# Kernel tuning notes

Measured on AMD Instinct MI355X. Metric: run time of the kernel, lower is better.

Reference implementation:

```python
import jax, jax.numpy as jnp
import numpy as np

N = 4096          # nodes (= Mamba sequence length)
E_EDGES = 65536   # edges
D = 512           # dim_h (= d_inner, expand=1)
NEXP = 4          # num_experts (cfg.model.num_experts)
DSTATE = 16
DCONV = 4
DTRANK = 32       # ceil(D/16)
EPS = 1e-5


def _silu(x):
    return x * jax.nn.sigmoid(x)


def _bn(h, g, b):
    # BatchNorm1d over node axis (batch statistics)
    mu = h.mean(0)
    var = h.var(0)
    return (h - mu) * jax.lax.rsqrt(var + EPS) * g + b


def _mamba(u, in_w, conv_w, conv_b, x_w, dt_w, dt_b, A_log, Dp, out_w):
    # u: [L, D] single-sequence Mamba(d_model=D, d_state=16, d_conv=4, expand=1)
    L = u.shape[0]
    xz = u @ in_w                      # [L, 2D]
    xc, z = xz[:, :D], xz[:, D:]
    xp = jnp.pad(xc, ((DCONV - 1, 0), (0, 0)))
    xconv = conv_b
    for k in range(DCONV):             # depthwise causal conv, tiny fixed loop
        xconv = xconv + conv_w[:, k] * xp[k:k + L]
    xs = _silu(xconv)                  # [L, D]
    dbc = xs @ x_w                     # [L, DTRANK + 2*DSTATE]
    dt = jax.nn.softplus(dbc[:, :DTRANK] @ dt_w + dt_b)          # [L, D]
    Bm = dbc[:, DTRANK:DTRANK + DSTATE]                          # [L, S]
    Cm = dbc[:, DTRANK + DSTATE:]                                # [L, S]
    A = -jnp.exp(A_log)                                          # [D, S]
    dA = jnp.exp(dt[:, :, None] * A[None])                       # [L, D, S]
    dBu = dt[:, :, None] * Bm[:, None, :] * xs[:, :, None]       # [L, D, S]

    def step(hprev, inp):
        dA_t, dBu_t, C_t = inp
        hn = dA_t * hprev + dBu_t
        return hn, (hn * C_t[None, :]).sum(-1)

    _, ys = jax.lax.scan(step, jnp.zeros((D, DSTATE), u.dtype), (dA, dBu, Cm))
    y = ys + Dp * xs
    return (y * _silu(z)) @ out_w      # [L, D]


def setup_inputs() -> dict:
    key = jax.random.key(0)
    ks = jax.random.split(key, 24)
    s = 1.0 / np.sqrt(D)
    inp = {}
    inp['x'] = jax.random.normal(ks[0], (N, D), jnp.float32)
    inp['edge_index'] = jax.random.randint(ks[1], (2, E_EDGES), 0, N)
    inp['edge_attr'] = jax.random.normal(ks[2], (E_EDGES, D), jnp.float32)
    # GINE nn: Linear(D,D) -> ReLU -> Linear(D,D)
    inp['gin_w1'] = jax.random.normal(ks[3], (D, D)) * s
    inp['gin_b1'] = jnp.zeros((D,))
    inp['gin_w2'] = jax.random.normal(ks[4], (D, D)) * s
    inp['gin_b2'] = jnp.zeros((D,))
    # BatchNorms
    inp['bn1l_g'] = jnp.ones((D,)); inp['bn1l_b'] = jnp.zeros((D,))
    inp['bn1a_g'] = jnp.ones((D,)); inp['bn1a_b'] = jnp.zeros((D,))
    inp['bn2_g'] = jnp.ones((D,)); inp['bn2_b'] = jnp.zeros((D,))
    # gating MLP [D, D//2, NEXP]
    inp['gate_w1'] = jax.random.normal(ks[5], (D, D // 2)) * s
    inp['gate_b1'] = jnp.zeros((D // 2,))
    inp['gate_w2'] = jax.random.normal(ks[6], (D // 2, NEXP)) * (1.0 / np.sqrt(D // 2))
    inp['gate_b2'] = jnp.zeros((NEXP,))
    # stacked per-expert Mamba params
    inp['in_w'] = jax.random.normal(ks[7], (NEXP, D, 2 * D)) * s
    inp['conv_w'] = jax.random.normal(ks[8], (NEXP, D, DCONV)) * 0.5
    inp['conv_b'] = jnp.zeros((NEXP, D))
    inp['x_w'] = jax.random.normal(ks[9], (NEXP, D, DTRANK + 2 * DSTATE)) * s
    inp['dt_w'] = jax.random.normal(ks[10], (NEXP, DTRANK, D)) * (1.0 / np.sqrt(DTRANK))
    inp['dt_b'] = jax.random.normal(ks[11], (NEXP, D)) * 0.1 - 4.0
    A0 = jnp.log(jnp.arange(1, DSTATE + 1, dtype=jnp.float32))
    inp['A_log'] = jnp.broadcast_to(A0, (NEXP, D, DSTATE)).copy()
    inp['Dp'] = jnp.ones((NEXP, D))
    inp['out_w'] = jax.random.normal(ks[12], (NEXP, D, D)) * s
    # FFN
    inp['ff_w1'] = jax.random.normal(ks[13], (D, 2 * D)) * s
    inp['ff_b1'] = jnp.zeros((2 * D,))
    inp['ff_w2'] = jax.random.normal(ks[14], (2 * D, D)) * (1.0 / np.sqrt(2 * D))
    inp['ff_b2'] = jnp.zeros((D,))
    return inp


def reference(x, edge_index, edge_attr,
              gin_w1, gin_b1, gin_w2, gin_b2,
              bn1l_g, bn1l_b, bn1a_g, bn1a_b, bn2_g, bn2_b,
              gate_w1, gate_b1, gate_w2, gate_b2,
              in_w, conv_w, conv_b, x_w, dt_w, dt_b, A_log, Dp, out_w,
              ff_w1, ff_b1, ff_w2, ff_b2):
    h_in = x
    src, dst = edge_index[0], edge_index[1]
    # local GINEConv: nn(x + sum_j relu(x_j + e_ji))
    msg = jax.nn.relu(x[src] + edge_attr)                      # [E, D]
    aggr = jax.ops.segment_sum(msg, dst, num_segments=N)       # [N, D]
    h_local = jax.nn.relu((x + aggr) @ gin_w1 + gin_b1) @ gin_w2 + gin_b2
    h_local = _bn(h_in + h_local, bn1l_g, bn1l_b)
    # gated mixture of Mamba experts
    gate = jax.nn.softmax(jax.nn.relu(x @ gate_w1 + gate_b1) @ gate_w2 + gate_b2, axis=-1)  # [N, NEXP]
    ys = jax.vmap(_mamba, in_axes=(None, 0, 0, 0, 0, 0, 0, 0, 0, 0))(
        x, in_w, conv_w, conv_b, x_w, dt_w, dt_b, A_log, Dp, out_w)  # [NEXP, N, D]
    h_attn = jnp.einsum('ne,end->nd', gate, ys)
    h_attn = _bn(h_in + h_attn, bn1a_g, bn1a_b)
    # fuse + FFN
    h = h_local + h_attn
    ff = jax.nn.relu(h @ ff_w1 + ff_b1) @ ff_w2 + ff_b2
    return _bn(h + ff, bn2_g, bn2_b)
```

## Files before the change

kernel.cpp:

```cpp
#include <hip/hip_runtime.h>
#include <hip/hip_bf16.h>
#include <math.h>

#define N_NODES 4096
#define E_EDGE 65536
#define D 512
#define NEXP 4
#define DSTATE 16
#define DCONV 4
#define DTRANK 32
#define EPS 1e-5f
#define LCHUNK 32
#define NCHUNK (N_NODES / LCHUNK)

typedef __hip_bfloat16 bf16;
typedef short bf16x8 __attribute__((ext_vector_type(8)));
typedef float f32x4 __attribute__((ext_vector_type(4)));
typedef unsigned short u16x4 __attribute__((ext_vector_type(4)));

__device__ __forceinline__ float siluf(float x) { return x / (1.f + __expf(-x)); }
__device__ __forceinline__ float softplusf(float x) {
  return (x > 20.f) ? x : log1pf(__expf(x));
}
__device__ __forceinline__ unsigned short f2bf(float v) {
  bf16 b = __float2bfloat16(v);
  return *reinterpret_cast<unsigned short*>(&b);
}
__device__ __forceinline__ float bfu2f(unsigned short u) {
  bf16 b;
  *reinterpret_cast<unsigned short*>(&b) = u;
  return __bfloat162float(b);
}

__device__ __forceinline__ void gload16(const void* g, void* l) {
  __builtin_amdgcn_global_load_lds(
      (const __attribute__((address_space(1))) void*)g,
      (__attribute__((address_space(3))) void*)l, 16, 0, 0);
}

template <int FN, int EPI, bool STATS>
__global__ __launch_bounds__(256, 2) void mm_k(
    const bf16* __restrict__ A, int lda, long sA,
    const bf16* __restrict__ Bt, int ldb, long sB,
    const float* __restrict__ bias,
    float* __restrict__ Cf, bf16* __restrict__ Cb, int ldc, long sC, int K,
    const float* __restrict__ part, float* __restrict__ sacc) {
  constexpr int BN = FN * 32;
  __shared__ __align__(16) bf16 As[2][128 * 32];
  __shared__ __align__(16) bf16 Bs[2][BN * 32];
  const int z = blockIdx.z;
  A += (size_t)z * sA;
  Bt += (size_t)z * sB;
  const int tid = threadIdx.x;
  const int w = tid >> 6, l = tid & 63;
  const int wr = w >> 1, wc = w & 1;
  const int bm = blockIdx.y * 128, bn = blockIdx.x * BN;

  f32x4 acc[4][FN];
#pragma unroll
  for (int i = 0; i < 4; ++i)
#pragma unroll
    for (int j = 0; j < FN; ++j) acc[i][j] = 0.f;

  const int srow = l >> 2, schunk = l & 3;
  const bf16* gA = A + (size_t)(bm + w * 16 + srow) * lda + schunk * 8;
  const bf16* gB = Bt + (size_t)(bn + w * 16 + srow) * ldb + schunk * 8;

  const int ar = wr * 64 + (l & 15);
  const int br = wc * FN * 16 + (l & 15);
  const int kb = l >> 4;

  auto stage = [&](int b, int k0) {
    gload16(gA + k0, As[b] + w * 512);
    gload16(gA + k0 + (size_t)64 * lda, As[b] + 64 * 32 + w * 512);
    gload16(gB + k0, Bs[b] + w * 512);
    if (FN == 4) gload16(gB + k0 + (size_t)64 * ldb, Bs[b] + 64 * 32 + w * 512);
  };

  stage(0, 0);
  __syncthreads();
  int cur = 0;
  for (int k0 = 0; k0 < K; k0 += 32) {
    if (k0 + 32 < K) stage(cur ^ 1, k0 + 32);
    const bf16x8* Ap = (const bf16x8*)As[cur];
    const bf16x8* Bp = (const bf16x8*)Bs[cur];
    bf16x8 af[4], bfr[FN];
#pragma unroll
    for (int i = 0; i < 4; ++i) af[i] = Ap[(ar + i * 16) * 4 + kb];
#pragma unroll
    for (int j = 0; j < FN; ++j) bfr[j] = Bp[(br + j * 16) * 4 + kb];
#pragma unroll
    for (int i = 0; i < 4; ++i)
#pragma unroll
      for (int j = 0; j < FN; ++j)
        acc[i][j] = __builtin_amdgcn_mfma_f32_16x16x32_bf16(bfr[j], af[i], acc[i][j], 0, 0, 0);
    __syncthreads();
    cur ^= 1;
  }

  if (Cf) Cf += (size_t)z * sC;
  if (Cb) Cb += (size_t)z * sC;
  const int r0 = bm + wr * 64 + (l & 15);
  const int cb0 = bn + wc * FN * 16 + ((l >> 4) << 2);
  f32x4 ssum[FN], ssq[FN];
  if (STATS) {
#pragma unroll
    for (int j = 0; j < FN; ++j) { ssum[j] = 0.f; ssq[j] = 0.f; }
  }
#pragma unroll
  for (int i = 0; i < 4; ++i) {
    const int row = r0 + i * 16;
#pragma unroll
    for (int j = 0; j < FN; ++j) {
      const int col = cb0 + j * 16;
      f32x4 v = acc[i][j];
      if (bias) v += *(const f32x4*)&bias[col];
      if (EPI == 1) {
#pragma unroll
        for (int r = 0; r < 4; ++r) v[r] = fmaxf(v[r], 0.f);
      }
      if (Cf) *(f32x4*)&Cf[(size_t)row * ldc + col] = v;
      if (Cb) {
        u16x4 u;
#pragma unroll
        for (int r = 0; r < 4; ++r) u[r] = f2bf(v[r]);
        *(u16x4*)&Cb[(size_t)row * ldc + col] = u;
      }
      if (STATS) {
        f32x4 p = *(const f32x4*)&part[(size_t)row * ldc + col];
        f32x4 t = v + p;
        ssum[j] += t;
        ssq[j] += t * t;
      }
    }
  }
  if (STATS) {
#pragma unroll
    for (int m = 1; m < 16; m <<= 1) {
#pragma unroll
      for (int j = 0; j < FN; ++j)
#pragma unroll
        for (int r = 0; r < 4; ++r) {
          ssum[j][r] += __shfl_xor(ssum[j][r], m);
          ssq[j][r] += __shfl_xor(ssq[j][r], m);
        }
    }
    if ((l & 15) == 0) {
#pragma unroll
      for (int j = 0; j < FN; ++j)
#pragma unroll
        for (int r = 0; r < 4; ++r) {
          atomicAdd(&sacc[cb0 + j * 16 + r], ssum[j][r]);
          atomicAdd(&sacc[512 + cb0 + j * 16 + r], ssq[j][r]);
        }
    }
  }
}

struct MmArgs {
  const bf16* A[4];
  const bf16* Bt[4];
  const float* bias[4];
  float* Cf[4];
  bf16* Cb[4];
  const float* part[4];
  float* sacc[4];
  long sA[4], sB[4], sC[4];
  int lda[4], ldb[4], ldc[4], K[4], epi[4], stats[4], gx[4], cum[4];
};
__global__ __launch_bounds__(256, 2) void mgemm_k(MmArgs a) {
  __shared__ __align__(16) bf16 As[2][128 * 32];
  __shared__ __align__(16) bf16 Bs[2][64 * 32];
  int b = blockIdx.x;
  int i = 0;
  while (b >= a.cum[i]) ++i;
  int local = b - (i ? a.cum[i - 1] : 0);
  const int perz = a.gx[i] * 32;
  const int z = local / perz;
  const int rem = local - z * perz;
  const int by = rem / a.gx[i];
  const int bx = rem - by * a.gx[i];
  const int lda = a.lda[i], ldb = a.ldb[i], ldc = a.ldc[i], K = a.K[i];
  const bf16* A = a.A[i] + (size_t)z * a.sA[i];
  const bf16* Bt = a.Bt[i] + (size_t)z * a.sB[i];

  const int tid = threadIdx.x;
  const int w = tid >> 6, l = tid & 63;
  const int wr = w >> 1, wc = w & 1;
  const int bm = by * 128, bn = bx * 64;

  f32x4 acc[4][2];
#pragma unroll
  for (int p = 0; p < 4; ++p)
#pragma unroll
    for (int j = 0; j < 2; ++j) acc[p][j] = 0.f;

  const int srow = l >> 2, schunk = l & 3;
  const bf16* gA = A + (size_t)(bm + w * 16 + srow) * lda + schunk * 8;
  const bf16* gB = Bt + (size_t)(bn + w * 16 + srow) * ldb + schunk * 8;

  const int ar = wr * 64 + (l & 15);
  const int br = wc * 32 + (l & 15);
  const int kb = l >> 4;

  auto stage = [&](int bb, int k0) {
    gload16(gA + k0, As[bb] + w * 512);
    gload16(gA + k0 + (size_t)64 * lda, As[bb] + 64 * 32 + w * 512);
    gload16(gB + k0, Bs[bb] + w * 512);
  };

  stage(0, 0);
  __syncthreads();
  int cur = 0;
  for (int k0 = 0; k0 < K; k0 += 32) {
    if (k0 + 32 < K) stage(cur ^ 1, k0 + 32);
    const bf16x8* Ap = (const bf16x8*)As[cur];
    const bf16x8* Bp = (const bf16x8*)Bs[cur];
    bf16x8 af[4], bfr[2];
#pragma unroll
    for (int p = 0; p < 4; ++p) af[p] = Ap[(ar + p * 16) * 4 + kb];
#pragma unroll
    for (int j = 0; j < 2; ++j) bfr[j] = Bp[(br + j * 16) * 4 + kb];
#pragma unroll
    for (int p = 0; p < 4; ++p)
#pragma unroll
      for (int j = 0; j < 2; ++j)
        acc[p][j] = __builtin_amdgcn_mfma_f32_16x16x32_bf16(bfr[j], af[p], acc[p][j], 0, 0, 0);
    __syncthreads();
    cur ^= 1;
  }

  float* Cf = a.Cf[i] ? a.Cf[i] + (size_t)z * a.sC[i] : nullptr;
  bf16* Cb = a.Cb[i] ? a.Cb[i] + (size_t)z * a.sC[i] : nullptr;
  const float* bias = a.bias[i];
  const int epi = a.epi[i], stats = a.stats[i];
  const int r0 = bm + wr * 64 + (l & 15);
  const int cb0 = bn + wc * 32 + ((l >> 4) << 2);
  f32x4 ssum[2], ssq[2];
  ssum[0] = 0.f; ssum[1] = 0.f; ssq[0] = 0.f; ssq[1] = 0.f;
#pragma unroll
  for (int p = 0; p < 4; ++p) {
    const int row = r0 + p * 16;
#pragma unroll
    for (int j = 0; j < 2; ++j) {
      const int col = cb0 + j * 16;
      f32x4 v = acc[p][j];
      if (bias) v += *(const f32x4*)&bias[col];
      if (epi == 1) {
#pragma unroll
        for (int r = 0; r < 4; ++r) v[r] = fmaxf(v[r], 0.f);
      }
      if (Cf) *(f32x4*)&Cf[(size_t)row * ldc + col] = v;
      if (Cb) {
        u16x4 u;
#pragma unroll
        for (int r = 0; r < 4; ++r) u[r] = f2bf(v[r]);
        *(u16x4*)&Cb[(size_t)row * ldc + col] = u;
      }
      if (stats) {
        f32x4 pp = *(const f32x4*)&a.part[i][(size_t)row * ldc + col];
        f32x4 t = v + pp;
        ssum[j] += t;
        ssq[j] += t * t;
      }
    }
  }
  if (stats) {
#pragma unroll
    for (int m = 1; m < 16; m <<= 1) {
#pragma unroll
      for (int j = 0; j < 2; ++j)
#pragma unroll
        for (int r = 0; r < 4; ++r) {
          ssum[j][r] += __shfl_xor(ssum[j][r], m);
          ssq[j][r] += __shfl_xor(ssq[j][r], m);
        }
    }
    if ((l & 15) == 0) {
#pragma unroll
      for (int j = 0; j < 2; ++j)
#pragma unroll
        for (int r = 0; r < 4; ++r) {
          atomicAdd(&a.sacc[i][cb0 + j * 16 + r], ssum[j][r]);
          atomicAdd(&a.sacc[i][512 + cb0 + j * 16 + r], ssq[j][r]);
        }
    }
  }
}

struct WtArgs {
  const float* in[8];
  bf16* out[8];
  int K[8], N[8], ldo[8];
  long sin[8], sout[8];
  int cum[8];
};
__global__ __launch_bounds__(256) void wtrans_all_k(WtArgs a) {
  __shared__ float t[32][33];
  int b = blockIdx.x;
  int i = 0;
  while (b >= a.cum[i]) ++i;
  int local = b - (i ? a.cum[i - 1] : 0);
  const int ntx = a.N[i] / 32;
  const int nty = a.K[i] / 32;
  const int perz = ntx * nty;
  const int z = local / perz;
  const int rem = local - z * perz;
  const int bx = rem % ntx, by = rem / ntx;
  const float* in = a.in[i] + (size_t)z * a.sin[i];
  bf16* out = a.out[i] + (size_t)z * a.sout[i];
  const int N = a.N[i], ldo = a.ldo[i];
  const int n0 = bx * 32, k0 = by * 32;
  const int tx = threadIdx.x & 31, ty = threadIdx.x >> 5;
  for (int r = ty; r < 32; r += 8) t[r][tx] = in[(size_t)(k0 + r) * N + n0 + tx];
  __syncthreads();
  for (int r = ty; r < 32; r += 8)
    out[(size_t)(n0 + r) * ldo + k0 + tx] = __float2bfloat16(t[tx][r]);
}

__global__ void hist_k(const int* __restrict__ ei, int* __restrict__ deg) {
  int e = blockIdx.x * 256 + threadIdx.x;
  if (e < E_EDGE) atomicAdd(&deg[ei[E_EDGE + e]], 1);
}

__global__ __launch_bounds__(1024) void prefix_k(const int* __restrict__ deg,
                                                 int* __restrict__ rowstart) {
  __shared__ int s[1024];
  int t = threadIdx.x;
  int base = t * 4;
  int d0 = deg[base], d1 = deg[base + 1], d2 = deg[base + 2], d3 = deg[base + 3];
  int sum = d0 + d1 + d2 + d3;
  s[t] = sum;
  __syncthreads();
  for (int off = 1; off < 1024; off <<= 1) {
    int v = (t >= off) ? s[t - off] : 0;
    __syncthreads();
    s[t] += v;
    __syncthreads();
  }
  int excl = s[t] - sum;
  rowstart[base] = excl;
  rowstart[base + 1] = excl + d0;
  rowstart[base + 2] = excl + d0 + d1;
  rowstart[base + 3] = excl + d0 + d1 + d2;
}

__global__ void scatter_k(const int* __restrict__ ei, const int* __restrict__ rowstart,
                          int* __restrict__ cnt, int* __restrict__ eid) {
  int e = blockIdx.x * 256 + threadIdx.x;
  if (e < E_EDGE) {
    int dst = ei[E_EDGE + e];
    int slot = rowstart[dst] + atomicAdd(&cnt[dst], 1);
    eid[slot] = e;
  }
}

__global__ __launch_bounds__(256) void aggr_gather_k(
    const float* __restrict__ x, const int* __restrict__ ei, const float* __restrict__ ea,
    const int* __restrict__ rowstart, const int* __restrict__ deg,
    const int* __restrict__ eid, bf16* __restrict__ hpre, bf16* __restrict__ xbf) {
  __shared__ float comb[512];
  const int n = blockIdx.x;
  const int sub = threadIdx.x >> 7;
  const int lane = threadIdx.x & 127;
  const int d4 = lane << 2;
  const int beg = rowstart[n];
  const int end = beg + deg[n];
  f32x4 a = 0.f;
  for (int i = beg + sub; i < end; i += 2) {
    const int e = eid[i];
    const int s = ei[e];
    f32x4 xv = *(const f32x4*)&x[(size_t)s * D + d4];
    f32x4 ev = *(const f32x4*)&ea[(size_t)e * D + d4];
#pragma unroll
    for (int j = 0; j < 4; ++j) a[j] += fmaxf(xv[j] + ev[j], 0.f);
  }
  if (sub == 0) *(f32x4*)&comb[d4] = a;
  __syncthreads();
  if (sub == 1) {
    a += *(const f32x4*)&comb[d4];
    f32x4 xn = *(const f32x4*)&x[(size_t)n * D + d4];
    u16x4 h, xb;
#pragma unroll
    for (int j = 0; j < 4; ++j) {
      h[j] = f2bf(xn[j] + a[j]);
      xb[j] = f2bf(xn[j]);
    }
    *(u16x4*)&hpre[(size_t)n * D + d4] = h;
    *(u16x4*)&xbf[(size_t)n * D + d4] = xb;
  }
}

__device__ __forceinline__ void gate2_body(const float* __restrict__ g1,
                                           const float* __restrict__ w2,
                                           const float* __restrict__ b2,
                                           float* __restrict__ gate, int blk) {
  int row = blk * 4 + (threadIdx.x >> 6);
  int lane = threadIdx.x & 63;
  float a0 = 0.f, a1 = 0.f, a2 = 0.f, a3 = 0.f;
  for (int k = lane; k < 256; k += 64) {
    float v = g1[(size_t)row * 256 + k];
    a0 = fmaf(v, w2[k * 4 + 0], a0);
    a1 = fmaf(v, w2[k * 4 + 1], a1);
    a2 = fmaf(v, w2[k * 4 + 2], a2);
    a3 = fmaf(v, w2[k * 4 + 3], a3);
  }
#pragma unroll
  for (int off = 32; off; off >>= 1) {
    a0 += __shfl_down(a0, off);
    a1 += __shfl_down(a1, off);
    a2 += __shfl_down(a2, off);
    a3 += __shfl_down(a3, off);
  }
  if (lane == 0) {
    float l0 = a0 + b2[0], l1 = a1 + b2[1], l2 = a2 + b2[2], l3 = a3 + b2[3];
    float m = fmaxf(fmaxf(l0, l1), fmaxf(l2, l3));
    float e0 = __expf(l0 - m), e1 = __expf(l1 - m), e2 = __expf(l2 - m), e3 = __expf(l3 - m);
    float s = 1.f / (e0 + e1 + e2 + e3);
    gate[row * 4 + 0] = e0 * s;
    gate[row * 4 + 1] = e1 * s;
    gate[row * 4 + 2] = e2 * s;
    gate[row * 4 + 3] = e3 * s;
  }
}

__global__ __launch_bounds__(256) void gate2_k(const float* __restrict__ g1,
                                               const float* __restrict__ w2,
                                               const float* __restrict__ b2,
                                               float* __restrict__ gate) {
  gate2_body(g1, w2, b2, gate, blockIdx.x);
}

__device__ __forceinline__ void conv_body(const bf16* __restrict__ xz,
                                          const float* __restrict__ cw,
                                          const float* __restrict__ cb,
                                          bf16* __restrict__ xs, int z, int e0, int bx) {
  xz += (size_t)z * N_NODES * 2 * D;
  xs += (size_t)z * N_NODES * D;
  cw += (size_t)(e0 + z) * D * DCONV;
  cb += (size_t)(e0 + z) * D;
  int idx = bx * 256 + threadIdx.x;
  if (idx >= N_NODES * (D / 4)) return;
  int t = idx >> 7;
  int d4 = (idx & 127) << 2;
  float a[4];
#pragma unroll
  for (int j = 0; j < 4; ++j) a[j] = cb[d4 + j];
#pragma unroll
  for (int k = 0; k < DCONV; ++k) {
    int tt = t + k - (DCONV - 1);
    if (tt >= 0) {
      u16x4 v = *(const u16x4*)&xz[(size_t)tt * (2 * D) + d4];
#pragma unroll
      for (int j = 0; j < 4; ++j) a[j] = fmaf(cw[(d4 + j) * DCONV + k], bfu2f(v[j]), a[j]);
    }
  }
  u16x4 o;
#pragma unroll
  for (int j = 0; j < 4; ++j) o[j] = f2bf(siluf(a[j]));
  *(u16x4*)&xs[(size_t)t * D + d4] = o;
}

__global__ void conv_silu_k(const bf16* __restrict__ xz, const float* __restrict__ cw,
                            const float* __restrict__ cb, bf16* __restrict__ xs, int e0) {
  conv_body(xz, cw, cb, xs, blockIdx.y, e0, blockIdx.x);
}

__global__ __launch_bounds__(256) void convgate_k(
    const bf16* __restrict__ xz, const float* __restrict__ cw,
    const float* __restrict__ cb, bf16* __restrict__ xs,
    const float* __restrict__ g1, const float* __restrict__ w2,
    const float* __restrict__ b2, float* __restrict__ gate) {
  if (blockIdx.y == 4) {
    if (blockIdx.x < N_NODES / 4) gate2_body(g1, w2, b2, gate, blockIdx.x);
    return;
  }
  conv_body(xz, cw, cb, xs, blockIdx.y, 0, blockIdx.x);
}

__global__ void dt_k(const float* __restrict__ dbc, const float* __restrict__ dtw,
                     const float* __restrict__ dtbias, bf16* __restrict__ dt, int e0) {
  const int z = blockIdx.y;
  dbc += (size_t)z * N_NODES * 64;
  dt += (size_t)z * N_NODES * D;
  dtw += (size_t)(e0 + z) * DTRANK * D;
  dtbias += (size_t)(e0 + z) * D;
  int idx = blockIdx.x * blockDim.x + threadIdx.x;
  if (idx >= N_NODES * (D / 4)) return;
  int t = idx >> 7;
  int d4 = (idx & 127) << 2;
  f32x4 a = *(const f32x4*)&dtbias[d4];
#pragma unroll
  for (int k = 0; k < DTRANK; ++k) {
    float b = dbc[t * 64 + k];
    f32x4 wv = *(const f32x4*)&dtw[k * D + d4];
    a += b * wv;
  }
  u16x4 o;
#pragma unroll
  for (int j = 0; j < 4; ++j) o[j] = f2bf(softplusf(a[j]));
  *(u16x4*)&dt[(size_t)t * D + d4] = o;
}

__device__ __forceinline__ void bn_params(const float* acc, int d, float& mu, float& rsig) {
  mu = acc[d] * (1.f / N_NODES);
  float var = acc[512 + d] * (1.f / N_NODES) - mu * mu;
  rsig = rsqrtf(var + EPS);
}

__global__ void norm_k(const float* __restrict__ p, const float* __restrict__ q,
                       const float* __restrict__ acc, const float* __restrict__ g,
                       const float* __restrict__ b, float* __restrict__ o) {
  int idx = blockIdx.x * blockDim.x + threadIdx.x;
  if (idx >= N_NODES * (D / 4)) return;
  int d4 = (idx & 127) << 2;
  size_t base = (size_t)idx << 2;
  f32x4 pv = *(const f32x4*)&p[base];
  f32x4 qv = *(const f32x4*)&q[base];
  f32x4 gv = *(const f32x4*)&g[d4];
  f32x4 bv = *(const f32x4*)&b[d4];
  f32x4 ov;
#pragma unroll
  for (int j = 0; j < 4; ++j) {
    float mu, rs;
    bn_params(acc, d4 + j, mu, rs);
    ov[j] = (pv[j] + qv[j] - mu) * rs * gv[j] + bv[j];
  }
  *(f32x4*)&o[base] = ov;
}

__global__ void bnadd2_k(const float* __restrict__ x, const float* __restrict__ hloc,
                         const float* __restrict__ hattn, const float* __restrict__ acc1,
                         const float* __restrict__ acc2, const float* __restrict__ g1,
                         const float* __restrict__ b1, const float* __restrict__ g2,
                         const float* __restrict__ b2, float* __restrict__ of,
                         bf16* __restrict__ ob) {
  int idx = blockIdx.x * blockDim.x + threadIdx.x;
  if (idx >= N_NODES * (D / 4)) return;
  int d4 = (idx & 127) << 2;
  size_t base = (size_t)idx << 2;
  f32x4 xv = *(const f32x4*)&x[base];
  f32x4 hl = *(const f32x4*)&hloc[base];
  f32x4 ha = *(const f32x4*)&hattn[base];
  f32x4 g1v = *(const f32x4*)&g1[d4];
  f32x4 b1v = *(const f32x4*)&b1[d4];
  f32x4 g2v = *(const f32x4*)&g2[d4];
  f32x4 b2v = *(const f32x4*)&b2[d4];
  f32x4 ov;
  u16x4 obv;
#pragma unroll
  for (int j = 0; j < 4; ++j) {
    float mu1, rs1, mu2, rs2;
    bn_params(acc1, d4 + j, mu1, rs1);
    bn_params(acc2, d4 + j, mu2, rs2);
    float v = (xv[j] + hl[j] - mu1) * rs1 * g1v[j] + b1v[j] +
              (xv[j] + ha[j] - mu2) * rs2 * g2v[j] + b2v[j];
    ov[j] = v;
    obv[j] = f2bf(v);
  }
  *(f32x4*)&of[base] = ov;
  *(u16x4*)&ob[base] = obv;
}

__global__ __launch_bounds__(512) void scanA_k(const bf16* __restrict__ dt,
                                               const bf16* __restrict__ xs,
                                               const float* __restrict__ dbc,
                                               const float* __restrict__ Alog,
                                               float* __restrict__ Q,
                                               float* __restrict__ dtsum, int e0) {
  const int z = blockIdx.y;
  dt += (size_t)z * N_NODES * D;
  xs += (size_t)z * N_NODES * D;
  dbc += (size_t)z * N_NODES * 64;
  Alog += (size_t)(e0 + z) * D * DSTATE;
  Q += (size_t)z * NCHUNK * D * DSTATE;
  dtsum += (size_t)z * NCHUNK * D;
  int c = blockIdx.x;
  int d = threadIdx.x;
  float As[DSTATE], h[DSTATE];
#pragma unroll
  for (int s = 0; s < DSTATE; ++s) {
    As[s] = -__expf(Alog[d * DSTATE + s]);
    h[s] = 0.f;
  }
  float dts = 0.f;
  int t0 = c * LCHUNK;
  for (int t = t0; t < t0 + LCHUNK; ++t) {
    float dtv = __bfloat162float(dt[(size_t)t * D + d]);
    float xv = __bfloat162float(xs[(size_t)t * D + d]);
    float bx = dtv * xv;
    dts += dtv;
#pragma unroll
    for (int s = 0; s < DSTATE; ++s) {
      float Bv = dbc[(size_t)t * 64 + DTRANK + s];
      h[s] = fmaf(__expf(dtv * As[s]), h[s], bx * Bv);
    }
  }
  size_t base = ((size_t)c * D + d) * DSTATE;
#pragma unroll
  for (int s = 0; s < DSTATE; ++s) Q[base + s] = h[s];
  dtsum[c * D + d] = dts;
}

__global__ __launch_bounds__(256) void scanB_k(const float* __restrict__ Q,
                                               const float* __restrict__ dtsum,
                                               const float* __restrict__ Alog,
                                               float* __restrict__ Hin, int e0) {
  const int z = blockIdx.y;
  Q += (size_t)z * NCHUNK * D * DSTATE;
  dtsum += (size_t)z * NCHUNK * D;
  Alog += (size_t)(e0 + z) * D * DSTATE;
  Hin += (size_t)z * NCHUNK * D * DSTATE;
  int idx = blockIdx.x * blockDim.x + threadIdx.x;
  int d = idx >> 4;
  float As = -__expf(Alog[idx]);
  float h = 0.f;
  for (int c = 0; c < NCHUNK; ++c) {
    size_t base = (size_t)c * D * DSTATE + idx;
    Hin[base] = h;
    h = fmaf(__expf(As * dtsum[c * D + d]), h, Q[base]);
  }
}

__global__ __launch_bounds__(512) void scanC_k(const bf16* __restrict__ dt,
                                               const bf16* __restrict__ xs,
                                               const float* __restrict__ dbc,
                                               const float* __restrict__ Alog,
                                               const float* __restrict__ Hin,
                                               const bf16* __restrict__ xz,
                                               const float* __restrict__ Dp,
                                               const float* __restrict__ gate,
                                               bf16* __restrict__ u, int e0) {
  const int z = blockIdx.y;
  dt += (size_t)z * N_NODES * D;
  xs += (size_t)z * N_NODES * D;
  dbc += (size_t)z * N_NODES * 64;
  Alog += (size_t)(e0 + z) * D * DSTATE;
  Hin += (size_t)z * NCHUNK * D * DSTATE;
  xz += (size_t)z * N_NODES * 2 * D;
  Dp += (size_t)(e0 + z) * D;
  u += (size_t)(e0 + z) * 512;
  const int ge = e0 + z;
  int c = blockIdx.x;
  int d = threadIdx.x;
  float As[DSTATE], h[DSTATE];
  size_t base = ((size_t)c * D + d) * DSTATE;
#pragma unroll
  for (int s = 0; s < DSTATE; ++s) {
    As[s] = -__expf(Alog[d * DSTATE + s]);
    h[s] = Hin[base + s];
  }
  float Dv = Dp[d];
  int t0 = c * LCHUNK;
  for (int t = t0; t < t0 + LCHUNK; ++t) {
    float dtv = __bfloat162float(dt[(size_t)t * D + d]);
    float xv = __bfloat162float(xs[(size_t)t * D + d]);
    float bx = dtv * xv;
    float y = 0.f;
#pragma unroll
    for (int s = 0; s < DSTATE; ++s) {
      float Bv = dbc[(size_t)t * 64 + DTRANK + s];
      float Cv = dbc[(size_t)t * 64 + DTRANK + DSTATE + s];
      h[s] = fmaf(__expf(dtv * As[s]), h[s], bx * Bv);
      y = fmaf(h[s], Cv, y);
    }
    float zv = __bfloat162float(xz[(size_t)t * (2 * D) + D + d]);
    float gv = gate[t * NEXP + ge];
    u[(size_t)t * 2048 + d] = __float2bfloat16(gv * (y + Dv * xv) * siluf(zv));
  }
}

extern "C" void kernel_launch(void* const* d_in, const int* in_sizes, int n_in,
                              void* d_out, int out_size, void* d_ws, size_t ws_size,
                              hipStream_t stream) {
  const float* x = (const float*)d_in[0];
  const int* ei = (const int*)d_in[1];
  const float* ea = (const float*)d_in[2];
  const float* gin_w1 = (const float*)d_in[3];
  const float* gin_b1 = (const float*)d_in[4];
  const float* gin_w2 = (const float*)d_in[5];
  const float* gin_b2 = (const float*)d_in[6];
  const float* bn1l_g = (const float*)d_in[7];
  const float* bn1l_b = (const float*)d_in[8];
  const float* bn1a_g = (const float*)d_in[9];
  const float* bn1a_b = (const float*)d_in[10];
  const float* bn2_g = (const float*)d_in[11];
  const float* bn2_b = (const float*)d_in[12];
  const float* gate_w1 = (const float*)d_in[13];
  const float* gate_b1 = (const float*)d_in[14];
  const float* gate_w2 = (const float*)d_in[15];
  const float* gate_b2 = (const float*)d_in[16];
  const float* in_w = (const float*)d_in[17];
  const float* conv_w = (const float*)d_in[18];
  const float* conv_b = (const float*)d_in[19];
  const float* x_w = (const float*)d_in[20];
  const float* dt_w = (const float*)d_in[21];
  const float* dt_b = (const float*)d_in[22];
  const float* A_log = (const float*)d_in[23];
  const float* Dp = (const float*)d_in[24];
  const float* out_w = (const float*)d_in[25];
  const float* ff_w1 = (const float*)d_in[26];
  const float* ff_b1 = (const float*)d_in[27];
  const float* ff_w2 = (const float*)d_in[28];
  const float* ff_b2 = (const float*)d_in[29];
  float* out = (float*)d_out;

  const size_t ND = (size_t)N_NODES * D;
  const size_t NDb = ND / 2;

  const size_t fixed_f = 3 * ND + (size_t)N_NODES * 256 + 16384 + 2490624 + ND + 2048 +
                         81920 + 2 * ND + 4096;
  const size_t per_f = 2 * ND + NDb + (size_t)N_NODES * 64 + NDb +
                       2 * (size_t)NCHUNK * D * DSTATE + (size_t)NCHUNK * D;
  const int EB = (ws_size >= (fixed_f + 4 * per_f + 65536) * sizeof(float)) ? 4 : 1;

  float* ws = (float*)d_ws;
  size_t off = 0;
  auto alloc = [&](size_t n) {
    float* p = ws + off;
    off += (n + 63) & ~(size_t)63;
    return p;
  };
  float* ffo = alloc(ND);
  float* pbuf = alloc(ND);
  float* hlocal = alloc(ND);
  float* g1 = alloc((size_t)N_NODES * 256);
  float* gate = alloc((size_t)N_NODES * NEXP);
  bf16* gw1t = (bf16*)alloc(131072);
  bf16* gw2t = (bf16*)alloc(131072);
  bf16* gatew1t = (bf16*)alloc(65536);
  bf16* inwt = (bf16*)alloc(1048576);
  bf16* xwt = (bf16*)alloc(65536);
  bf16* outwt_cat = (bf16*)alloc(524288);
  bf16* ffw1t = (bf16*)alloc(262144);
  bf16* ffw2t = (bf16*)alloc(262144);
  int* deg = (int*)alloc(N_NODES);
  int* cnt = (int*)alloc(N_NODES);
  float* accs = alloc(3072);
  int* eid = (int*)alloc(E_EDGE);
  int* rowstart = (int*)alloc(N_NODES);
  float* xbf_f = alloc(NDb);
  float* xz_f = alloc((size_t)EB * ND);
  float* xs_f = alloc((size_t)EB * NDb);
  float* dbc = alloc((size_t)EB * N_NODES * 64);
  float* dtb_f = alloc((size_t)EB * NDb);
  float* Qb = alloc((size_t)EB * NCHUNK * D * DSTATE);
  float* Hin = alloc((size_t)EB * NCHUNK * D * DSTATE);
  float* dtsum = alloc((size_t)EB * NCHUNK * D);
  float* ucat_f = alloc(4 * NDb);
  float* hattn_raw = alloc(ND);
  float* acc1 = accs, *acc2 = accs + 1024, *acc3 = accs + 2048;

  bf16* x_bf = (bf16*)xbf_f;
  bf16* hpre_bf = (bf16*)pbuf;
  bf16* t1_bf = (bf16*)(pbuf + NDb);
  bf16* xz_bf = (bf16*)xz_f;
  bf16* xs_bf = (bf16*)xs_f;
  bf16* dt_bf = (bf16*)dtb_f;
  bf16* ucat = (bf16*)ucat_f;
  float* hcomb = xz_f;
  bf16* hcomb_bf = (bf16*)(ucat_f);
  bf16* ffh_bf = (bf16*)pbuf;

  const int nelem = N_NODES * D;
  const int ew4 = (nelem / 4 + 255) / 256;

  hipMemsetAsync(deg, 0, (N_NODES + N_NODES + 3072) * sizeof(float), stream);

  WtArgs wa;
  const float* wsrc[8] = {gin_w1, gin_w2, gate_w1, in_w, x_w, out_w, ff_w1, ff_w2};
  bf16* wdst[8] = {gw1t, gw2t, gatew1t, inwt, xwt, outwt_cat, ffw1t, ffw2t};
  int wK[8] = {512, 512, 512, 512, 512, 512, 512, 1024};
  int wN[8] = {512, 512, 256, 1024, 64, 512, 1024, 512};
  int wldo[8] = {512, 512, 512, 512, 512, 2048, 512, 1024};
  long wsin[8] = {0, 0, 0, (long)512 * 1024, (long)512 * 64, (long)512 * 512, 0, 0};
  long wsout[8] = {0, 0, 0, (long)512 * 1024, (long)64 * 512, 512, 0, 0};
  int wz[8] = {1, 1, 1, 4, 4, 4, 1, 1};
  int cum = 0;
  for (int i = 0; i < 8; ++i) {
    wa.in[i] = wsrc[i];
    wa.out[i] = wdst[i];
    wa.K[i] = wK[i];
    wa.N[i] = wN[i];
    wa.ldo[i] = wldo[i];
    wa.sin[i] = wsin[i];
    wa.sout[i] = wsout[i];
    cum += (wN[i] / 32) * (wK[i] / 32) * wz[i];
    wa.cum[i] = cum;
  }
  wtrans_all_k<<<cum, 256, 0, stream>>>(wa);

  hist_k<<<E_EDGE / 256, 256, 0, stream>>>(ei, deg);
  prefix_k<<<1, 1024, 0, stream>>>(deg, rowstart);
  scatter_k<<<E_EDGE / 256, 256, 0, stream>>>(ei, rowstart, cnt, eid);
  aggr_gather_k<<<N_NODES, 256, 0, stream>>>(x, ei, ea, rowstart, deg, eid, hpre_bf, x_bf);

  if (EB == 4) {
    MmArgs m1 = {};
    m1.A[0] = hpre_bf; m1.lda[0] = 512; m1.sA[0] = 0;
    m1.Bt[0] = gw1t; m1.ldb[0] = 512; m1.sB[0] = 0;
    m1.bias[0] = gin_b1; m1.Cb[0] = t1_bf; m1.ldc[0] = 512; m1.sC[0] = 0;
    m1.K[0] = 512; m1.epi[0] = 1; m1.gx[0] = 8;
    m1.A[1] = x_bf; m1.lda[1] = 512; m1.sA[1] = 0;
    m1.Bt[1] = gatew1t; m1.ldb[1] = 512; m1.sB[1] = 0;
    m1.bias[1] = gate_b1; m1.Cf[1] = g1; m1.ldc[1] = 256; m1.sC[1] = 0;
    m1.K[1] = 512; m1.epi[1] = 1; m1.gx[1] = 4;
    m1.A[2] = x_bf; m1.lda[2] = 512; m1.sA[2] = 0;
    m1.Bt[2] = inwt; m1.ldb[2] = 512; m1.sB[2] = (long)512 * 1024;
    m1.Cb[2] = xz_bf; m1.ldc[2] = 1024; m1.sC[2] = (long)N_NODES * 1024;
    m1.K[2] = 512; m1.epi[2] = 0; m1.gx[2] = 16;
    int c1 = 8 * 32;
    m1.cum[0] = c1;
    c1 += 4 * 32;
    m1.cum[1] = c1;
    c1 += 16 * 32 * 4;
    m1.cum[2] = c1;
    m1.cum[3] = c1;
    mgemm_k<<<c1, 256, 0, stream>>>(m1);
    convgate_k<<<dim3(ew4, 5), 256, 0, stream>>>(xz_bf, conv_w, conv_b, xs_bf, g1,
                                                 gate_w2, gate_b2, gate);

    MmArgs m2 = {};
    m2.A[0] = t1_bf; m2.lda[0] = 512; m2.sA[0] = 0;
    m2.Bt[0] = gw2t; m2.ldb[0] = 512; m2.sB[0] = 0;
    m2.bias[0] = gin_b2; m2.Cf[0] = hlocal; m2.ldc[0] = 512; m2.sC[0] = 0;
    m2.K[0] = 512; m2.epi[0] = 0; m2.stats[0] = 1; m2.part[0] = x; m2.sacc[0] = acc1;
    m2.gx[0] = 8;
    m2.A[1] = xs_bf; m2.lda[1] = 512; m2.sA[1] = (long)ND;
    m2.Bt[1] = xwt; m2.ldb[1] = 512; m2.sB[1] = (long)64 * 512;
    m2.Cf[1] = dbc; m2.ldc[1] = 64; m2.sC[1] = (long)N_NODES * 64;
    m2.K[1] = 512; m2.epi[1] = 0; m2.gx[1] = 1;
    int c2 = 8 * 32;
    m2.cum[0] = c2;
    c2 += 1 * 32 * 4;
    m2.cum[1] = c2;
    m2.cum[2] = c2;
    m2.cum[3] = c2;
    mgemm_k<<<c2, 256, 0, stream>>>(m2);

    dt_k<<<dim3(ew4, 4), 256, 0, stream>>>(dbc, dt_w, dt_b, dt_bf, 0);
    scanA_k<<<dim3(NCHUNK, 4), 512, 0, stream>>>(dt_bf, xs_bf, dbc, A_log, Qb, dtsum, 0);
    scanB_k<<<dim3((D * DSTATE) / 256, 4), 256, 0, stream>>>(Qb, dtsum, A_log, Hin, 0);
    scanC_k<<<dim3(NCHUNK, 4), 512, 0, stream>>>(dt_bf, xs_bf, dbc, A_log, Hin, xz_bf, Dp,
                                                 gate, ucat, 0);
  } else {
    mm_k<2, 1, false><<<dim3(8, 32, 1), 256, 0, stream>>>(
        hpre_bf, 512, 0, gw1t, 512, 0, gin_b1, nullptr, t1_bf, 512, 0, 512, nullptr,
        nullptr);
    mm_k<2, 0, true><<<dim3(8, 32, 1), 256, 0, stream>>>(
        t1_bf, 512, 0, gw2t, 512, 0, gin_b2, hlocal, nullptr, 512, 0, 512, x, acc1);
    mm_k<2, 1, false><<<dim3(4, 32, 1), 256, 0, stream>>>(
        x_bf, 512, 0, gatew1t, 512, 0, gate_b1, g1, nullptr, 256, 0, 512, nullptr,
        nullptr);
    gate2_k<<<N_NODES / 4, 256, 0, stream>>>(g1, gate_w2, gate_b2, gate);
    for (int e0 = 0; e0 < NEXP; ++e0) {
      mm_k<4, 0, false><<<dim3(8, 32, 1), 256, 0, stream>>>(
          x_bf, 512, 0, inwt + (size_t)e0 * 512 * 1024, 512, 0, nullptr, nullptr, xz_bf,
          1024, 0, 512, nullptr, nullptr);
      conv_silu_k<<<dim3(ew4, 1), 256, 0, stream>>>(xz_bf, conv_w, conv_b, xs_bf, e0);
      mm_k<2, 0, false><<<dim3(1, 32, 1), 256, 0, stream>>>(
          xs_bf, 512, 0, xwt + (size_t)e0 * 64 * 512, 512, 0, nullptr, dbc, nullptr, 64,
          0, 512, nullptr, nullptr);
      dt_k<<<dim3(ew4, 1), 256, 0, stream>>>(dbc, dt_w, dt_b, dt_bf, e0);
      scanA_k<<<dim3(NCHUNK, 1), 512, 0, stream>>>(dt_bf, xs_bf, dbc, A_log, Qb, dtsum, e0);
      scanB_k<<<dim3((D * DSTATE) / 256, 1), 256, 0, stream>>>(Qb, dtsum, A_log, Hin, e0);
      scanC_k<<<dim3(NCHUNK, 1), 512, 0, stream>>>(dt_bf, xs_bf, dbc, A_log, Hin, xz_bf,
                                                   Dp, gate, ucat, e0);
    }
  }

  mm_k<2, 0, true><<<dim3(8, 32, 1), 256, 0, stream>>>(
      ucat, 2048, 0, outwt_cat, 2048, 0, nullptr, hattn_raw, nullptr, 512, 0, 2048, x,
      acc2);

  bnadd2_k<<<ew4, 256, 0, stream>>>(x, hlocal, hattn_raw, acc1, acc2, bn1l_g, bn1l_b,
                                    bn1a_g, bn1a_b, hcomb, hcomb_bf);
  mm_k<4, 1, false><<<dim3(8, 32, 1), 256, 0, stream>>>(
      hcomb_bf, 512, 0, ffw1t, 512, 0, ff_b1, nullptr, ffh_bf, 1024, 0, 512, nullptr,
      nullptr);
  mm_k<2, 0, true><<<dim3(8, 32, 1), 256, 0, stream>>>(
      ffh_bf, 1024, 0, ffw2t, 1024, 0, ff_b2, ffo, nullptr, 512, 0, 1024, hcomb, acc3);
  norm_k<<<ew4, 256, 0, stream>>>(hcomb, ffo, acc3, bn2_g, bn2_b, out);
}
```

Measured before the change: 459.7 us.

## Fuse dt projection into scanA and store GEMM outputs as bf16

Removes the separate dt_k kernel by computing the dt low-rank projection and softplus inside scanA. Each thread keeps its 32 dt weights in registers and writes the bf16 dt for scanC to reuse. Separately, the pre-BatchNorm outputs of the GIN, Mamba-out and FFN2 GEMMs are now stored as bf16, halving their write and read traffic in the norm kernels. The cost is extra serial work and register pressure in scanA, plus reduced precision in the intermediates that feed BatchNorm. The batch statistics are still accumulated in fp32 inside the GEMM epilogues.

```diff
diff --git a/kernel.cpp b/kernel.cpp
--- a/kernel.cpp
+++ b/kernel.cpp
@@ -478,37 +478,13 @@
   conv_body(xz, cw, cb, xs, blockIdx.y, 0, blockIdx.x);
 }
 
-__global__ void dt_k(const float* __restrict__ dbc, const float* __restrict__ dtw,
-                     const float* __restrict__ dtbias, bf16* __restrict__ dt, int e0) {
-  const int z = blockIdx.y;
-  dbc += (size_t)z * N_NODES * 64;
-  dt += (size_t)z * N_NODES * D;
-  dtw += (size_t)(e0 + z) * DTRANK * D;
-  dtbias += (size_t)(e0 + z) * D;
-  int idx = blockIdx.x * blockDim.x + threadIdx.x;
-  if (idx >= N_NODES * (D / 4)) return;
-  int t = idx >> 7;
-  int d4 = (idx & 127) << 2;
-  f32x4 a = *(const f32x4*)&dtbias[d4];
-#pragma unroll
-  for (int k = 0; k < DTRANK; ++k) {
-    float b = dbc[t * 64 + k];
-    f32x4 wv = *(const f32x4*)&dtw[k * D + d4];
-    a += b * wv;
-  }
-  u16x4 o;
-#pragma unroll
-  for (int j = 0; j < 4; ++j) o[j] = f2bf(softplusf(a[j]));
-  *(u16x4*)&dt[(size_t)t * D + d4] = o;
-}
-
 __device__ __forceinline__ void bn_params(const float* acc, int d, float& mu, float& rsig) {
   mu = acc[d] * (1.f / N_NODES);
   float var = acc[512 + d] * (1.f / N_NODES) - mu * mu;
   rsig = rsqrtf(var + EPS);
 }
 
-__global__ void norm_k(const float* __restrict__ p, const float* __restrict__ q,
+__global__ void norm_k(const float* __restrict__ p, const bf16* __restrict__ q,
                        const float* __restrict__ acc, const float* __restrict__ g,
                        const float* __restrict__ b, float* __restrict__ o) {
   int idx = blockIdx.x * blockDim.x + threadIdx.x;
@@ -516,7 +492,7 @@
   int d4 = (idx & 127) << 2;
   size_t base = (size_t)idx << 2;
   f32x4 pv = *(const f32x4*)&p[base];
-  f32x4 qv = *(const f32x4*)&q[base];
+  u16x4 qv = *(const u16x4*)&q[base];
   f32x4 gv = *(const f32x4*)&g[d4];
   f32x4 bv = *(const f32x4*)&b[d4];
   f32x4 ov;
@@ -524,13 +500,13 @@
   for (int j = 0; j < 4; ++j) {
     float mu, rs;
     bn_params(acc, d4 + j, mu, rs);
-    ov[j] = (pv[j] + qv[j] - mu) * rs * gv[j] + bv[j];
+    ov[j] = (pv[j] + bfu2f(qv[j]) - mu) * rs * gv[j] + bv[j];
   }
   *(f32x4*)&o[base] = ov;
 }
 
-__global__ void bnadd2_k(const float* __restrict__ x, const float* __restrict__ hloc,
-                         const float* __restrict__ hattn, const float* __restrict__ acc1,
+__global__ void bnadd2_k(const float* __restrict__ x, const bf16* __restrict__ hloc,
+                         const bf16* __restrict__ hattn, const float* __restrict__ acc1,
                          const float* __restrict__ acc2, const float* __restrict__ g1,
                          const float* __restrict__ b1, const float* __restrict__ g2,
                          const float* __restrict__ b2, float* __restrict__ of,
@@ -540,8 +516,8 @@
   int d4 = (idx & 127) << 2;
   size_t base = (size_t)idx << 2;
   f32x4 xv = *(const f32x4*)&x[base];
-  f32x4 hl = *(const f32x4*)&hloc[base];
-  f32x4 ha = *(const f32x4*)&hattn[base];
+  u16x4 hl = *(const u16x4*)&hloc[base];
+  u16x4 ha = *(const u16x4*)&hattn[base];
   f32x4 g1v = *(const f32x4*)&g1[d4];
   f32x4 b1v = *(const f32x4*)&b1[d4];
   f32x4 g2v = *(const f32x4*)&g2[d4];
@@ -553,8 +529,8 @@
     float mu1, rs1, mu2, rs2;
     bn_params(acc1, d4 + j, mu1, rs1);
     bn_params(acc2, d4 + j, mu2, rs2);
-    float v = (xv[j] + hl[j] - mu1) * rs1 * g1v[j] + b1v[j] +
-              (xv[j] + ha[j] - mu2) * rs2 * g2v[j] + b2v[j];
+    float v = (xv[j] + bfu2f(hl[j]) - mu1) * rs1 * g1v[j] + b1v[j] +
+              (xv[j] + bfu2f(ha[j]) - mu2) * rs2 * g2v[j] + b2v[j];
     ov[j] = v;
     obv[j] = f2bf(v);
   }
@@ -562,21 +538,29 @@
   *(u16x4*)&ob[base] = obv;
 }
 
-__global__ __launch_bounds__(512) void scanA_k(const bf16* __restrict__ dt,
-                                               const bf16* __restrict__ xs,
+__global__ __launch_bounds__(512) void scanA_k(const bf16* __restrict__ xs,
                                                const float* __restrict__ dbc,
                                                const float* __restrict__ Alog,
+                                               const float* __restrict__ dtw,
+                                               const float* __restrict__ dtbias,
+                                               bf16* __restrict__ dtout,
                                                float* __restrict__ Q,
                                                float* __restrict__ dtsum, int e0) {
   const int z = blockIdx.y;
-  dt += (size_t)z * N_NODES * D;
   xs += (size_t)z * N_NODES * D;
   dbc += (size_t)z * N_NODES * 64;
   Alog += (size_t)(e0 + z) * D * DSTATE;
+  dtw += (size_t)(e0 + z) * DTRANK * D;
+  dtbias += (size_t)(e0 + z) * D;
+  dtout += (size_t)z * N_NODES * D;
   Q += (size_t)z * NCHUNK * D * DSTATE;
   dtsum += (size_t)z * NCHUNK * D;
   int c = blockIdx.x;
   int d = threadIdx.x;
+  float wv[DTRANK];
+#pragma unroll
+  for (int k = 0; k < DTRANK; ++k) wv[k] = dtw[k * D + d];
+  const float dtb0 = dtbias[d];
   float As[DSTATE], h[DSTATE];
 #pragma unroll
   for (int s = 0; s < DSTATE; ++s) {
@@ -586,7 +570,12 @@
   float dts = 0.f;
   int t0 = c * LCHUNK;
   for (int t = t0; t < t0 + LCHUNK; ++t) {
-    float dtv = __bfloat162float(dt[(size_t)t * D + d]);
+    float acc = dtb0;
+#pragma unroll
+    for (int k = 0; k < DTRANK; ++k) acc = fmaf(dbc[(size_t)t * 64 + k], wv[k], acc);
+    bf16 dtb16 = __float2bfloat16(softplusf(acc));
+    dtout[(size_t)t * D + d] = dtb16;
+    float dtv = __bfloat162float(dtb16);
     float xv = __bfloat162float(xs[(size_t)t * D + d]);
     float bx = dtv * xv;
     dts += dtv;
@@ -721,9 +710,9 @@
     off += (n + 63) & ~(size_t)63;
     return p;
   };
-  float* ffo = alloc(ND);
+  float* ffo_f = alloc(ND);
   float* pbuf = alloc(ND);
-  float* hlocal = alloc(ND);
+  float* hlocal_f = alloc(ND);
   float* g1 = alloc((size_t)N_NODES * 256);
   float* gate = alloc((size_t)N_NODES * NEXP);
   bf16* gw1t = (bf16*)alloc(131072);
@@ -748,7 +737,7 @@
   float* Hin = alloc((size_t)EB * NCHUNK * D * DSTATE);
   float* dtsum = alloc((size_t)EB * NCHUNK * D);
   float* ucat_f = alloc(4 * NDb);
-  float* hattn_raw = alloc(ND);
+  float* hattn_f = alloc(ND);
   float* acc1 = accs, *acc2 = accs + 1024, *acc3 = accs + 2048;
 
   bf16* x_bf = (bf16*)xbf_f;
@@ -758,6 +747,9 @@
   bf16* xs_bf = (bf16*)xs_f;
   bf16* dt_bf = (bf16*)dtb_f;
   bf16* ucat = (bf16*)ucat_f;
+  bf16* hlocal_bf = (bf16*)hlocal_f;
+  bf16* hattn_bf = (bf16*)hattn_f;
+  bf16* ffo_bf = (bf16*)ffo_f;
   float* hcomb = xz_f;
   bf16* hcomb_bf = (bf16*)(ucat_f);
   bf16* ffh_bf = (bf16*)pbuf;
@@ -823,7 +815,7 @@
     MmArgs m2 = {};
     m2.A[0] = t1_bf; m2.lda[0] = 512; m2.sA[0] = 0;
     m2.Bt[0] = gw2t; m2.ldb[0] = 512; m2.sB[0] = 0;
-    m2.bias[0] = gin_b2; m2.Cf[0] = hlocal; m2.ldc[0] = 512; m2.sC[0] = 0;
+    m2.bias[0] = gin_b2; m2.Cb[0] = hlocal_bf; m2.ldc[0] = 512; m2.sC[0] = 0;
     m2.K[0] = 512; m2.epi[0] = 0; m2.stats[0] = 1; m2.part[0] = x; m2.sacc[0] = acc1;
     m2.gx[0] = 8;
     m2.A[1] = xs_bf; m2.lda[1] = 512; m2.sA[1] = (long)ND;
@@ -838,8 +830,8 @@
     m2.cum[3] = c2;
     mgemm_k<<<c2, 256, 0, stream>>>(m2);
 
-    dt_k<<<dim3(ew4, 4), 256, 0, stream>>>(dbc, dt_w, dt_b, dt_bf, 0);
-    scanA_k<<<dim3(NCHUNK, 4), 512, 0, stream>>>(dt_bf, xs_bf, dbc, A_log, Qb, dtsum, 0);
+    scanA_k<<<dim3(NCHUNK, 4), 512, 0, stream>>>(xs_bf, dbc, A_log, dt_w, dt_b, dt_bf,
+                                                 Qb, dtsum, 0);
     scanB_k<<<dim3((D * DSTATE) / 256, 4), 256, 0, stream>>>(Qb, dtsum, A_log, Hin, 0);
     scanC_k<<<dim3(NCHUNK, 4), 512, 0, stream>>>(dt_bf, xs_bf, dbc, A_log, Hin, xz_bf, Dp,
                                                  gate, ucat, 0);
@@ -848,7 +840,7 @@
         hpre_bf, 512, 0, gw1t, 512, 0, gin_b1, nullptr, t1_bf, 512, 0, 512, nullptr,
         nullptr);
     mm_k<2, 0, true><<<dim3(8, 32, 1), 256, 0, stream>>>(
-        t1_bf, 512, 0, gw2t, 512, 0, gin_b2, hlocal, nullptr, 512, 0, 512, x, acc1);
+        t1_bf, 512, 0, gw2t, 512, 0, gin_b2, nullptr, hlocal_bf, 512, 0, 512, x, acc1);
     mm_k<2, 1, false><<<dim3(4, 32, 1), 256, 0, stream>>>(
         x_bf, 512, 0, gatew1t, 512, 0, gate_b1, g1, nullptr, 256, 0, 512, nullptr,
         nullptr);
@@ -861,8 +853,8 @@
       mm_k<2, 0, false><<<dim3(1, 32, 1), 256, 0, stream>>>(
           xs_bf, 512, 0, xwt + (size_t)e0 * 64 * 512, 512, 0, nullptr, dbc, nullptr, 64,
           0, 512, nullptr, nullptr);
-      dt_k<<<dim3(ew4, 1), 256, 0, stream>>>(dbc, dt_w, dt_b, dt_bf, e0);
-      scanA_k<<<dim3(NCHUNK, 1), 512, 0, stream>>>(dt_bf, xs_bf, dbc, A_log, Qb, dtsum, e0);
+      scanA_k<<<dim3(NCHUNK, 1), 512, 0, stream>>>(xs_bf, dbc, A_log, dt_w, dt_b, dt_bf,
+                                                   Qb, dtsum, e0);
       scanB_k<<<dim3((D * DSTATE) / 256, 1), 256, 0, stream>>>(Qb, dtsum, A_log, Hin, e0);
       scanC_k<<<dim3(NCHUNK, 1), 512, 0, stream>>>(dt_bf, xs_bf, dbc, A_log, Hin, xz_bf,
                                                    Dp, gate, ucat, e0);
@@ -870,15 +862,15 @@
   }
 
   mm_k<2, 0, true><<<dim3(8, 32, 1), 256, 0, stream>>>(
-      ucat, 2048, 0, outwt_cat, 2048, 0, nullptr, hattn_raw, nullptr, 512, 0, 2048, x,
+      ucat, 2048, 0, outwt_cat, 2048, 0, nullptr, nullptr, hattn_bf, 512, 0, 2048, x,
       acc2);
 
-  bnadd2_k<<<ew4, 256, 0, stream>>>(x, hlocal, hattn_raw, acc1, acc2, bn1l_g, bn1l_b,
+  bnadd2_k<<<ew4, 256, 0, stream>>>(x, hlocal_bf, hattn_bf, acc1, acc2, bn1l_g, bn1l_b,
                                     bn1a_g, bn1a_b, hcomb, hcomb_bf);
   mm_k<4, 1, false><<<dim3(8, 32, 1), 256, 0, stream>>>(
       hcomb_bf, 512, 0, ffw1t, 512, 0, ff_b1, nullptr, ffh_bf, 1024, 0, 512, nullptr,
       nullptr);
   mm_k<2, 0, true><<<dim3(8, 32, 1), 256, 0, stream>>>(
-      ffh_bf, 1024, 0, ffw2t, 1024, 0, ff_b2, ffo, nullptr, 512, 0, 1024, hcomb, acc3);
-  norm_k<<<ew4, 256, 0, stream>>>(hcomb, ffo, acc3, bn2_g, bn2_b, out);
-}
+      ffh_bf, 1024, 0, ffw2t, 1024, 0, ff_b2, nullptr, ffo_bf, 512, 0, 1024, hcomb, acc3);
+  norm_k<<<ew4, 256, 0, stream>>>(hcomb, ffo_bf, acc3, bn2_g, bn2_b, out);
+}
```

New measurement: 429.6 us. 1.07x faster.
